# Kernel tuning notes

Hardware: AMD Instinct MI355X
Metric: run time of the kernel (lower is better)

## Reference

```python
import jax, jax.numpy as jnp
import numpy as np

N_NODES = 50000
EMBED_DIM = 512
N_EDGES = 150000


def _edge_scores(node_embeddings, edges):
    # edges: [2, E] int; dot product of endpoint embeddings -> [E]
    src = node_embeddings[edges[0]]  # [E, D]
    dst = node_embeddings[edges[1]]  # [E, D]
    return jnp.sum(src * dst, axis=1)


def setup_inputs() -> dict:
    key = jax.random.key(0)
    k1, k2, k3 = jax.random.split(key, 3)
    node_embeddings = jax.random.normal(k1, (N_NODES, EMBED_DIM), dtype=jnp.float32)
    edge_index = jax.random.randint(k2, (2, N_EDGES), 0, N_NODES, dtype=jnp.int64)
    # negative edges: uniform random node pairs (matches the original sampler's
    # fallback distribution; precomputed so the reference is deterministic/jittable)
    neg_edges = jax.random.randint(k3, (2, N_EDGES), 0, N_NODES, dtype=jnp.int64)
    return {
        "node_embeddings": node_embeddings,
        "edge_index": edge_index,
        "neg_edges": neg_edges,
        "num_nodes": N_NODES,
    }


def reference(node_embeddings, edge_index, neg_edges, num_nodes):
    pos_scores = _edge_scores(node_embeddings, edge_index)  # [E]
    neg_scores = _edge_scores(node_embeddings, neg_edges)   # [E]
    all_scores = jnp.concatenate([pos_scores, neg_scores])
    all_labels = jnp.concatenate([
        jnp.ones_like(pos_scores),
        jnp.zeros_like(neg_scores),
    ])
    # BCE with logits: log(1 + exp(s)) - s*y, numerically stable via logaddexp
    per_elem = jnp.logaddexp(jnp.float32(0.0), all_scores) - all_scores * all_labels
    return jnp.mean(per_elem)
```

## Files before the change

kernel.cpp:

```cpp
#include <hip/hip_runtime.h>
#include <math.h>

#define N_EDGES   150000
#define TOTAL     300000
#define EMBED_DIM 512
#define N_NODES   50000
#define TABLE_ELEMS (N_NODES * EMBED_DIM)
#define TABLE_BYTES_F8 ((size_t)TABLE_ELEMS)
#define BLOCK_THREADS 256
#define CONV_BLOCKS 2048

#define GROUPS16   (TOTAL / 16)
#define POS_G16    (N_EDGES / 16)
#define EDGE_BLOCKS ((GROUPS16 + 3) / 4)

typedef float floatx4 __attribute__((ext_vector_type(4)));
typedef unsigned long long ull;
typedef ull ull2 __attribute__((ext_vector_type(2)));

__global__ __launch_bounds__(BLOCK_THREADS) void convert_fp8(
    const float4* __restrict__ in,
    int*          __restrict__ out,
    float*        __restrict__ acc)
{
    if (blockIdx.x == 0 && threadIdx.x == 0) *acc = 0.0f;
    const int stride = gridDim.x * blockDim.x;
    for (int i = blockIdx.x * blockDim.x + threadIdx.x;
         i < TABLE_ELEMS / 4; i += stride) {
        float4 v = in[i];
        int r = 0;
        r = __builtin_amdgcn_cvt_pk_fp8_f32(v.x, v.y, r, false);
        r = __builtin_amdgcn_cvt_pk_fp8_f32(v.z, v.w, r, true);
        out[i] = r;
    }
}

__global__ __launch_bounds__(BLOCK_THREADS, 4) void edge_loss_fp8(
    const unsigned char* __restrict__ emb8,
    const int*           __restrict__ pos_edges,
    const int*           __restrict__ neg_edges,
    float*               __restrict__ acc)
{
    const int wave = threadIdx.x >> 6;
    const int lane = threadIdx.x & 63;
    const int g    = blockIdx.x * 4 + wave;

    const int i    = lane & 15;
    const int quad = lane >> 4;
    const bool is_diag = ((i >> 2) == quad);
    const int  dreg    = i & 3;

    float contrib = 0.0f;

    if (g < GROUPS16) {
        const bool is_pos = (g < POS_G16);
        const int* __restrict__ edges = is_pos ? pos_edges : neg_edges;
        const int  e0 = 16 * g - (is_pos ? 0 : N_EDGES);

        const int sidx = edges[e0 + i];
        const int tidx = edges[N_EDGES + e0 + i];

        const ull2* rA = (const ull2*)(emb8 + (size_t)sidx * EMBED_DIM + quad * 16);
        const ull2* rB = (const ull2*)(emb8 + (size_t)tidx * EMBED_DIM + quad * 16);

        ull2 a[8], b[8];
        #pragma unroll
        for (int c = 0; c < 8; c++) {
            a[c] = rA[c * 4];
            b[c] = rB[c * 4];
        }
#if __has_builtin(__builtin_amdgcn_sched_barrier)
        __builtin_amdgcn_sched_barrier(0);
#endif

        floatx4 C0 = {0,0,0,0}, C1 = {0,0,0,0}, C2 = {0,0,0,0}, C3 = {0,0,0,0};
        #pragma unroll
        for (int c = 0; c < 2; c++) {
            #pragma unroll
            for (int h = 0; h < 2; h++) {
                C0 = __builtin_amdgcn_mfma_f32_16x16x32_fp8_fp8((long)a[c][h],     (long)b[c][h],     C0, 0, 0, 0);
                C1 = __builtin_amdgcn_mfma_f32_16x16x32_fp8_fp8((long)a[2 + c][h], (long)b[2 + c][h], C1, 0, 0, 0);
                C2 = __builtin_amdgcn_mfma_f32_16x16x32_fp8_fp8((long)a[4 + c][h], (long)b[4 + c][h], C2, 0, 0, 0);
                C3 = __builtin_amdgcn_mfma_f32_16x16x32_fp8_fp8((long)a[6 + c][h], (long)b[6 + c][h], C3, 0, 0, 0);
            }
        }
        floatx4 C = (C0 + C1) + (C2 + C3);

        float s = (dreg == 0) ? C[0] : (dreg == 1) ? C[1] : (dreg == 2) ? C[2] : C[3];
        float sp = fmaxf(s, 0.0f) + log1pf(expf(-fabsf(s)));
        contrib = is_diag ? (sp - (is_pos ? s : 0.0f)) : 0.0f;
    }

    #pragma unroll
    for (int off = 32; off > 0; off >>= 1)
        contrib += __shfl_down(contrib, off, 64);

    __shared__ float ls[4];
    if (lane == 0) ls[wave] = contrib;
    __syncthreads();
    if (threadIdx.x == 0)
        atomicAdd(acc, ls[0] + ls[1] + ls[2] + ls[3]);
}

#define N_PAIRS   (TOTAL / 2)
#define POS_PAIRS (N_EDGES / 2)
#define FB_WAVES  (CONV_BLOCKS * 4)
__global__ __launch_bounds__(BLOCK_THREADS, 8) void edge_loss_f32(
    const float* __restrict__ emb,
    const int*   __restrict__ pos_edges,
    const int*   __restrict__ neg_edges,
    float*       __restrict__ acc)
{
    const int wave  = threadIdx.x >> 6;
    const int lane  = threadIdx.x & 63;
    const int gwave = blockIdx.x * 4 + wave;
    float lsum = 0.0f;
    for (int g = gwave; g < N_PAIRS; g += FB_WAVES) {
        const bool is_pos = (g < POS_PAIRS);
        const int* __restrict__ edges = is_pos ? pos_edges : neg_edges;
        const int  e0 = 2 * g - (is_pos ? 0 : N_EDGES);
        const int s0 = edges[e0],     t0 = edges[N_EDGES + e0];
        const int s1 = edges[e0 + 1], t1 = edges[N_EDGES + e0 + 1];
        const float4* rS0 = (const float4*)(emb + (size_t)s0 * EMBED_DIM) + lane;
        const float4* rT0 = (const float4*)(emb + (size_t)t0 * EMBED_DIM) + lane;
        const float4* rS1 = (const float4*)(emb + (size_t)s1 * EMBED_DIM) + lane;
        const float4* rT1 = (const float4*)(emb + (size_t)t1 * EMBED_DIM) + lane;
        float4 a0 = rS0[0], a1 = rS0[64];
        float4 b0 = rT0[0], b1 = rT0[64];
        float4 c0 = rS1[0], c1 = rS1[64];
        float4 d0 = rT1[0], d1 = rT1[64];
        float p0 = fmaf(a0.x, b0.x, fmaf(a0.y, b0.y, fmaf(a0.z, b0.z, a0.w * b0.w)));
        float p1 = fmaf(a1.x, b1.x, fmaf(a1.y, b1.y, fmaf(a1.z, b1.z, a1.w * b1.w)));
        float q0 = fmaf(c0.x, d0.x, fmaf(c0.y, d0.y, fmaf(c0.z, d0.z, c0.w * d0.w)));
        float q1 = fmaf(c1.x, d1.x, fmaf(c1.y, d1.y, fmaf(c1.z, d1.z, c1.w * d1.w)));
        float p = p0 + p1, q = q0 + q1;
        #pragma unroll
        for (int off = 32; off > 0; off >>= 1) {
            p += __shfl_down(p, off, 64);
            q += __shfl_down(q, off, 64);
        }
        const float sp_p = fmaxf(p, 0.0f) + log1pf(expf(-fabsf(p)));
        const float sp_q = fmaxf(q, 0.0f) + log1pf(expf(-fabsf(q)));
        lsum += (lane == 0) ? (sp_p + sp_q - (is_pos ? (p + q) : 0.0f)) : 0.0f;
    }
    __shared__ float ls[4];
    if (lane == 0) ls[wave] = lsum;
    __syncthreads();
    if (threadIdx.x == 0)
        atomicAdd(acc, ls[0] + ls[1] + ls[2] + ls[3]);
}

__global__ void finalize_kernel(const float* __restrict__ acc, float* __restrict__ out)
{
    if (threadIdx.x == 0)
        out[0] = acc[0] * (1.0f / (float)TOTAL);
}

extern "C" void kernel_launch(void* const* d_in, const int* in_sizes, int n_in,
                              void* d_out, int out_size, void* d_ws, size_t ws_size,
                              hipStream_t stream) {
    const float* emb = (const float*)d_in[0];
    const int*   pos = (const int*)d_in[1];
    const int*   neg = (const int*)d_in[2];
    float* out = (float*)d_out;

    if (ws_size >= TABLE_BYTES_F8 + 64) {
        unsigned char* emb8 = (unsigned char*)d_ws;
        float*         acc  = (float*)((char*)d_ws + TABLE_BYTES_F8);
        convert_fp8<<<CONV_BLOCKS, BLOCK_THREADS, 0, stream>>>(
            (const float4*)emb, (int*)d_ws, acc);
        edge_loss_fp8<<<EDGE_BLOCKS, BLOCK_THREADS, 0, stream>>>(emb8, pos, neg, acc);
        finalize_kernel<<<1, 64, 0, stream>>>(acc, out);
    } else {
        float* acc = (float*)d_ws;
        (void)hipMemsetAsync(acc, 0, sizeof(float), stream);
        edge_loss_f32<<<CONV_BLOCKS, BLOCK_THREADS, 0, stream>>>(emb, pos, neg, acc);
        finalize_kernel<<<1, 64, 0, stream>>>(acc, out);
    }
}
```

Measured before the change: 225.0 us.

## Split fp8 table into 64-byte dimension slices and score edges per slice

The fp8 conversion now writes the table as eight dimension-chunk slices of 3.2 MB each. The scoring kernel assigns blocks to slices (blockIdx & 7), so each slice's blocks gather rows from a working set small enough to stay cache-resident. Each wave writes per-chunk partial dot products to a workspace buffer. A new reduction kernel sums the eight partials per edge, applies the BCE term and finishes the mean with a last-block counter, which removes the separate finalize launch. In exchange the path writes and rereads a 9.6 MB partial buffer, needs a larger workspace, and falls back to the old path if the workspace is too small.

```diff
diff --git a/kernel.cpp b/kernel.cpp
--- a/kernel.cpp
+++ b/kernel.cpp
@@ -12,11 +12,118 @@
 
 #define GROUPS16   (TOTAL / 16)
 #define POS_G16    (N_EDGES / 16)
-#define EDGE_BLOCKS ((GROUPS16 + 3) / 4)
+
+#define NCHUNK       8
+#define CHUNK_BYTES  64
+#define SLICE_BYTES  ((size_t)N_NODES * CHUNK_BYTES)
+#define PARTIAL_BYTES ((size_t)NCHUNK * TOTAL * 4)
+#define WS_ACC_OFF   (TABLE_BYTES_F8 + PARTIAL_BYTES)
+#define WS_NEEDED    (WS_ACC_OFF + 64)
+
+#define SCORE_BLOCKS 2048
+#define BLOCKS_PER_CHUNK (SCORE_BLOCKS / NCHUNK)
+#define WAVES_PER_CHUNK  (BLOCKS_PER_CHUNK * 4)
+#define RED_BLOCKS ((TOTAL + BLOCK_THREADS - 1) / BLOCK_THREADS)
 
 typedef float floatx4 __attribute__((ext_vector_type(4)));
 typedef unsigned long long ull;
 typedef ull ull2 __attribute__((ext_vector_type(2)));
+
+__global__ __launch_bounds__(BLOCK_THREADS) void convert_fp8_chunked(
+    const float4* __restrict__ in,
+    int*          __restrict__ out,
+    float*        __restrict__ acc,
+    unsigned int* __restrict__ cnt)
+{
+    if (blockIdx.x == 0 && threadIdx.x == 0) { *acc = 0.0f; *cnt = 0u; }
+    const int stride = gridDim.x * blockDim.x;
+    for (int i = blockIdx.x * blockDim.x + threadIdx.x;
+         i < TABLE_ELEMS / 4; i += stride) {
+        float4 v = in[i];
+        int r = 0;
+        r = __builtin_amdgcn_cvt_pk_fp8_f32(v.x, v.y, r, false);
+        r = __builtin_amdgcn_cvt_pk_fp8_f32(v.z, v.w, r, true);
+        const int node  = i >> 7;
+        const int dim4  = i & 127;
+        const int chunk = dim4 >> 4;
+        const int w4    = dim4 & 15;
+        out[(size_t)chunk * (N_NODES * 16) + (size_t)node * 16 + w4] = r;
+    }
+}
+
+__global__ __launch_bounds__(BLOCK_THREADS, 8) void edge_score_chunked(
+    const unsigned char* __restrict__ emb8,
+    const int*           __restrict__ pos_edges,
+    const int*           __restrict__ neg_edges,
+    float*               __restrict__ partial)
+{
+    const int wave  = threadIdx.x >> 6;
+    const int lane  = threadIdx.x & 63;
+    const int chunk = blockIdx.x & 7;
+    const int w     = (blockIdx.x >> 3) * 4 + wave;
+
+    const int i    = lane & 15;
+    const int quad = lane >> 4;
+    const bool is_diag = ((i >> 2) == quad);
+    const int  dreg    = i & 3;
+
+    const unsigned char* __restrict__ slice = emb8 + (size_t)chunk * SLICE_BYTES;
+    float* __restrict__ pout = partial + (size_t)chunk * TOTAL;
+
+    for (int g = w; g < GROUPS16; g += WAVES_PER_CHUNK) {
+        const bool is_pos = (g < POS_G16);
+        const int* __restrict__ edges = is_pos ? pos_edges : neg_edges;
+        const int  e0a = 16 * g - (is_pos ? 0 : N_EDGES);
+
+        const int sidx = __builtin_nontemporal_load(edges + e0a + i);
+        const int tidx = __builtin_nontemporal_load(edges + N_EDGES + e0a + i);
+
+        const ull2 a = *(const ull2*)(slice + (size_t)(unsigned)sidx * CHUNK_BYTES + quad * 16);
+        const ull2 b = *(const ull2*)(slice + (size_t)(unsigned)tidx * CHUNK_BYTES + quad * 16);
+
+        floatx4 C = {0, 0, 0, 0};
+        C = __builtin_amdgcn_mfma_f32_16x16x32_fp8_fp8((long)a[0], (long)b[0], C, 0, 0, 0);
+        C = __builtin_amdgcn_mfma_f32_16x16x32_fp8_fp8((long)a[1], (long)b[1], C, 0, 0, 0);
+
+        const float s = (dreg == 0) ? C[0] : (dreg == 1) ? C[1] : (dreg == 2) ? C[2] : C[3];
+        if (is_diag)
+            __builtin_nontemporal_store(s, pout + 16 * g + i);
+    }
+}
+
+__global__ __launch_bounds__(BLOCK_THREADS) void reduce_bce_finalize(
+    const float*  __restrict__ partial,
+    float*        __restrict__ acc,
+    unsigned int* __restrict__ cnt,
+    float*        __restrict__ out)
+{
+    const int e = blockIdx.x * BLOCK_THREADS + threadIdx.x;
+    float term = 0.0f;
+    if (e < TOTAL) {
+        float s = 0.0f;
+        #pragma unroll
+        for (int c = 0; c < NCHUNK; c++)
+            s += partial[(size_t)c * TOTAL + e];
+        const float sp = fmaxf(s, 0.0f) + log1pf(expf(-fabsf(s)));
+        term = sp - (e < N_EDGES ? s : 0.0f);
+    }
+    #pragma unroll
+    for (int off = 32; off > 0; off >>= 1)
+        term += __shfl_down(term, off, 64);
+    __shared__ float ls[4];
+    if ((threadIdx.x & 63) == 0) ls[threadIdx.x >> 6] = term;
+    __syncthreads();
+    if (threadIdx.x == 0) {
+        atomicAdd(acc, ls[0] + ls[1] + ls[2] + ls[3]);
+        __threadfence();
+        const unsigned prev = atomicAdd(cnt, 1u);
+        if (prev == (unsigned)(gridDim.x - 1)) {
+            __threadfence();
+            const float tot = atomicAdd(acc, 0.0f);
+            out[0] = tot * (1.0f / (float)TOTAL);
+        }
+    }
+}
 
 __global__ __launch_bounds__(BLOCK_THREADS) void convert_fp8(
     const float4* __restrict__ in,
@@ -35,6 +142,7 @@
     }
 }
 
+#define EDGE_BLOCKS ((GROUPS16 + 3) / 4)
 __global__ __launch_bounds__(BLOCK_THREADS, 4) void edge_loss_fp8(
     const unsigned char* __restrict__ emb8,
     const int*           __restrict__ pos_edges,
@@ -44,35 +152,25 @@
     const int wave = threadIdx.x >> 6;
     const int lane = threadIdx.x & 63;
     const int g    = blockIdx.x * 4 + wave;
-
     const int i    = lane & 15;
     const int quad = lane >> 4;
     const bool is_diag = ((i >> 2) == quad);
     const int  dreg    = i & 3;
-
     float contrib = 0.0f;
-
     if (g < GROUPS16) {
         const bool is_pos = (g < POS_G16);
         const int* __restrict__ edges = is_pos ? pos_edges : neg_edges;
         const int  e0 = 16 * g - (is_pos ? 0 : N_EDGES);
-
         const int sidx = edges[e0 + i];
         const int tidx = edges[N_EDGES + e0 + i];
-
         const ull2* rA = (const ull2*)(emb8 + (size_t)sidx * EMBED_DIM + quad * 16);
         const ull2* rB = (const ull2*)(emb8 + (size_t)tidx * EMBED_DIM + quad * 16);
-
         ull2 a[8], b[8];
         #pragma unroll
-        for (int c = 0; c < 8; c++) {
-            a[c] = rA[c * 4];
-            b[c] = rB[c * 4];
-        }
+        for (int c = 0; c < 8; c++) { a[c] = rA[c * 4]; b[c] = rB[c * 4]; }
 #if __has_builtin(__builtin_amdgcn_sched_barrier)
         __builtin_amdgcn_sched_barrier(0);
 #endif
-
         floatx4 C0 = {0,0,0,0}, C1 = {0,0,0,0}, C2 = {0,0,0,0}, C3 = {0,0,0,0};
         #pragma unroll
         for (int c = 0; c < 2; c++) {
@@ -85,16 +183,13 @@
             }
         }
         floatx4 C = (C0 + C1) + (C2 + C3);
-
         float s = (dreg == 0) ? C[0] : (dreg == 1) ? C[1] : (dreg == 2) ? C[2] : C[3];
         float sp = fmaxf(s, 0.0f) + log1pf(expf(-fabsf(s)));
         contrib = is_diag ? (sp - (is_pos ? s : 0.0f)) : 0.0f;
     }
-
     #pragma unroll
     for (int off = 32; off > 0; off >>= 1)
         contrib += __shfl_down(contrib, off, 64);
-
     __shared__ float ls[4];
     if (lane == 0) ls[wave] = contrib;
     __syncthreads();
@@ -164,7 +259,18 @@
     const int*   neg = (const int*)d_in[2];
     float* out = (float*)d_out;
 
-    if (ws_size >= TABLE_BYTES_F8 + 64) {
+    if (ws_size >= WS_NEEDED) {
+        unsigned char* emb8    = (unsigned char*)d_ws;
+        float*         partial = (float*)((char*)d_ws + TABLE_BYTES_F8);
+        float*         acc     = (float*)((char*)d_ws + WS_ACC_OFF);
+        unsigned int*  cnt     = (unsigned int*)((char*)d_ws + WS_ACC_OFF + 4);
+        convert_fp8_chunked<<<CONV_BLOCKS, BLOCK_THREADS, 0, stream>>>(
+            (const float4*)emb, (int*)d_ws, acc, cnt);
+        edge_score_chunked<<<SCORE_BLOCKS, BLOCK_THREADS, 0, stream>>>(
+            emb8, pos, neg, partial);
+        reduce_bce_finalize<<<RED_BLOCKS, BLOCK_THREADS, 0, stream>>>(
+            partial, acc, cnt, out);
+    } else if (ws_size >= TABLE_BYTES_F8 + 64) {
         unsigned char* emb8 = (unsigned char*)d_ws;
         float*         acc  = (float*)((char*)d_ws + TABLE_BYTES_F8);
         convert_fp8<<<CONV_BLOCKS, BLOCK_THREADS, 0, stream>>>(
```

Measured after the change: 243.7 us. 1.08x slower.
